# Kernel optimization log

Hardware: AMD Instinct MI355X
Metric: run time of the kernel (lower is better)

The kernel has to match this reference:

```python
import jax, jax.numpy as jnp
import numpy as np

L, D, HID, NH, E, K, P, IMG, NC, B = 4, 384, 1536, 6, 8, 2, 16, 224, 1000, 8
S = (IMG // P) ** 2 + 1  # 197 tokens (cls + patches)
EPS = 1e-5


def setup_inputs() -> dict:
    ks = iter(jax.random.split(jax.random.key(0), 32))
    g = lambda shape, s=0.02: jax.random.normal(next(ks), shape, jnp.float32) * s
    pd = 3 * P * P
    return dict(
        x=jax.random.normal(next(ks), (B, 3, IMG, IMG), jnp.float32),
        patch_w=g((pd, D)), patch_b=g((D,)),
        cls_tok=g((1, 1, D)), pos=g((1, S, D)),
        qkv_w=g((L, D, 3 * D)), qkv_b=g((L, 3 * D)),
        proj_w=g((L, D, D)), proj_b=g((L, D)),
        ln1_g=jnp.ones((L, D)), ln1_b=jnp.zeros((L, D)),
        ln2_g=jnp.ones((L, D)), ln2_b=jnp.zeros((L, D)),
        router_w=g((L, D, E)), router_b=g((L, E)),
        w1=g((L, E, D, HID)), b1=g((L, E, HID)),
        w2=g((L, E, HID, D)), b2=g((L, E, D)),
        norm_g=jnp.ones((D,)), norm_b=jnp.zeros((D,)),
        fc_w=g((D, NC)), fc_b=g((NC,)),
    )


def _ln(x, g, b):
    m = x.mean(-1, keepdims=True)
    v = ((x - m) ** 2).mean(-1, keepdims=True)
    return (x - m) * jax.lax.rsqrt(v + EPS) * g + b


def _mha(x, wqkv, bqkv, wo, bo):
    Bx, Sx, Dx = x.shape
    hd = Dx // NH
    qkv = x @ wqkv + bqkv
    q, k, v = jnp.split(qkv, 3, axis=-1)
    q = q.reshape(Bx, Sx, NH, hd)
    k = k.reshape(Bx, Sx, NH, hd)
    v = v.reshape(Bx, Sx, NH, hd)
    att = jnp.einsum('bqhd,bkhd->bhqk', q, k) / jnp.sqrt(jnp.float32(hd))
    att = jax.nn.softmax(att, axis=-1)
    o = jnp.einsum('bhqk,bkhd->bqhd', att, v).reshape(Bx, Sx, Dx)
    return o @ wo + bo


def _moe(x, rw, rb, w1, b1, w2, b2, noise):
    # Faithful to the masked-dense SparseMoE: non-routed experts see zeros,
    # so occupied experts leak expert_j(0)=gelu(b1_j)@W2_j+b2_j to all tokens.
    xf = x.reshape(-1, x.shape[-1])                     # [T, D]
    logits = xf @ rw + rb + noise * 0.01                # noisy gating
    vals, idx = jax.lax.top_k(logits, K)                # [T, K]
    gates = jax.nn.softmax(vals, axis=-1)               # [T, K]
    h = jax.nn.gelu(jnp.einsum('td,edh->teh', xf, w1) + b1[None], approximate=False)
    y = jnp.einsum('teh,ehd->ted', h, w2) + b2[None]    # [T, E, D]
    bias0 = jnp.einsum('eh,ehd->ed', jax.nn.gelu(b1, approximate=False), w2) + b2  # expert_j(0)
    oh = jax.nn.one_hot(idx, E, dtype=xf.dtype)         # [T, K, E]
    occ = (oh.sum(0) > 0).astype(xf.dtype)              # [K, E] slot occupancy (mask.sum()>0)
    bias_sum = occ @ bias0                              # [K, D]
    y_sel = jnp.take_along_axis(y, idx[:, :, None], axis=1)  # [T, K, D]
    out = jnp.einsum('tk,tkd->td', gates, y_sel - bias0[idx] + bias_sum[None])
    return out.reshape(x.shape)


def reference(x, patch_w, patch_b, cls_tok, pos, qkv_w, qkv_b, proj_w, proj_b,
              ln1_g, ln1_b, ln2_g, ln2_b, router_w, router_b,
              w1, b1, w2, b2, norm_g, norm_b, fc_w, fc_b):
    Bx = x.shape[0]
    Hp = IMG // P
    # torch unfold patchify: (B,C,Hp,Wp,p,p) -> (B, N, C*p*p), channel-major features
    patches = x.reshape(Bx, 3, Hp, P, Hp, P).transpose(0, 2, 4, 1, 3, 5).reshape(Bx, Hp * Hp, 3 * P * P)
    t = patches @ patch_w + patch_b
    t = jnp.concatenate([jnp.broadcast_to(cls_tok, (Bx, 1, D)), t], axis=1) + pos
    nkey = jax.random.key(42)
    for l in range(L):
        a = _mha(t, qkv_w[l], qkv_b[l], proj_w[l], proj_b[l])
        t = _ln(t + a, ln1_g[l], ln1_b[l])
        noise = jax.random.normal(jax.random.fold_in(nkey, l), (Bx * S, E), t.dtype)
        m = _moe(t, router_w[l], router_b[l], w1[l], b1[l], w2[l], b2[l], noise)
        t = _ln(t + m, ln2_g[l], ln2_b[l])
    t = _ln(t, norm_g, norm_b)
    return t[:, 0] @ fc_w + fc_b
```

## Files before the change

### kernel.cpp

```cpp
#include <hip/hip_runtime.h>
#include <hip/hip_bf16.h>

constexpr int LYR  = 4;
constexpr int DM   = 384;
constexpr int HIDN = 1536;
constexpr int NHEAD = 6;
constexpr int HDIM = 64;
constexpr int NEXP = 8;
constexpr int SEQ  = 197;
constexpr int BATCH = 8;
constexpr int TOK  = BATCH * SEQ;
constexpr int NCLS = 1000;
constexpr int CAPE = TOK;
constexpr int NPATCH = BATCH * 196;
constexpr float EPSLN = 1e-5f;
constexpr int KP = 40;

typedef __attribute__((ext_vector_type(8))) short short8v;
typedef __attribute__((ext_vector_type(4))) short short4v;
typedef __attribute__((ext_vector_type(2))) short short2v;
typedef __attribute__((ext_vector_type(4))) float f32x4v;

__host__ __device__ inline void tf2x32(unsigned k0, unsigned k1, unsigned x0, unsigned x1,
                                       unsigned& y0, unsigned& y1) {
  unsigned ks2 = k0 ^ k1 ^ 0x1BD11BDAu;
  unsigned v0 = x0 + k0, v1 = x1 + k1;
#define TFR(r) { v0 += v1; v1 = (v1 << (r)) | (v1 >> (32 - (r))); v1 ^= v0; }
  TFR(13) TFR(15) TFR(26) TFR(6)
  v0 += k1;  v1 += ks2 + 1u;
  TFR(17) TFR(29) TFR(16) TFR(24)
  v0 += ks2; v1 += k0 + 2u;
  TFR(13) TFR(15) TFR(26) TFR(6)
  v0 += k0;  v1 += k1 + 3u;
  TFR(17) TFR(29) TFR(16) TFR(24)
  v0 += k1;  v1 += ks2 + 4u;
  TFR(13) TFR(15) TFR(26) TFR(6)
  v0 += ks2; v1 += k0 + 5u;
#undef TFR
  y0 = v0; y1 = v1;
}

__device__ inline float erfinv32(float x) {
  float w = -log1pf(-x * x);
  float p;
  if (w < 5.f) {
    w -= 2.5f;
    p = 2.81022636e-08f;
    p = fmaf(p, w, 3.43273939e-07f);
    p = fmaf(p, w, -3.5233877e-06f);
    p = fmaf(p, w, -4.39150654e-06f);
    p = fmaf(p, w, 0.00021858087f);
    p = fmaf(p, w, -0.00125372503f);
    p = fmaf(p, w, -0.00417768164f);
    p = fmaf(p, w, 0.246640727f);
    p = fmaf(p, w, 1.50140941f);
  } else {
    w = sqrtf(w) - 3.f;
    p = -0.000200214257f;
    p = fmaf(p, w, 0.000100950558f);
    p = fmaf(p, w, 0.00134934322f);
    p = fmaf(p, w, -0.00367342844f);
    p = fmaf(p, w, 0.00573950773f);
    p = fmaf(p, w, -0.0076224613f);
    p = fmaf(p, w, 0.00943887047f);
    p = fmaf(p, w, 1.00167406f);
    p = fmaf(p, w, 2.83297682f);
  }
  return p * x;
}

__device__ inline float gelu_f(float x) {
  return 0.5f * x * (1.f + erff(x * 0.70710678118654752f));
}

__device__ inline unsigned short bf16_rne(float x) {
  unsigned u = __float_as_uint(x);
  unsigned r = (u + 0x7fffu + ((u >> 16) & 1u)) >> 16;
  return (unsigned short)r;
}
__device__ inline void split2(float x, short& hs, short& ls) {
  unsigned hu = bf16_rne(x);
  float hf = __uint_as_float(hu << 16);
  unsigned lu = bf16_rne(x - hf);
  hs = (short)hu; ls = (short)lu;
}

__global__ __launch_bounds__(256) void convw_kernel(const float* __restrict__ src,
                                                    short* __restrict__ dst,
                                                    int K, int N,
                                                    long srcLS, long dstLS) {
  const int nrg = N >> 6;
  const int rg = blockIdx.x;
  const int kr = rg / nrg, nr = rg - kr * nrg;
  const long eoffS = (long)blockIdx.z * srcLS + (long)blockIdx.y * K * N;
  const int nchunks = (K >> 5) * (N >> 4);
  const long eoffD = (long)blockIdx.z * dstLS + (long)blockIdx.y * (long)nchunks * 1024;
  __shared__ float st[64][65];
  const int tid = threadIdx.x;
  {
    const int c = (tid & 15) << 2;
    const int r0 = tid >> 4;
    const float* sp = src + eoffS + (long)(kr * 64) * N + nr * 64;
#pragma unroll
    for (int p = 0; p < 4; ++p) {
      const int r = p * 16 + r0;
      const float4 v = *(const float4*)&sp[(long)r * N + c];
      st[r][c] = v.x; st[r][c + 1] = v.y; st[r][c + 2] = v.z; st[r][c + 3] = v.w;
    }
  }
  __syncthreads();
  const int lane = tid & 63;
  const int wch = tid >> 6;
  const int nloc0 = lane & 15, kg = lane >> 4;
#pragma unroll
  for (int q = 0; q < 2; ++q) {
    const int ch = wch + q * 4;
    const int kt2 = ch >> 2, nt2 = ch & 3;
    const int kl = kt2 * 32 + kg * 8;
    const int nl = nt2 * 16 + nloc0;
    short8v hv, lv;
#pragma unroll
    for (int j = 0; j < 8; j++) {
      short h, l; split2(st[kl + j][nl], h, l);
      hv[j] = h; lv[j] = l;
    }
    const int ktg = kr * 2 + kt2, ntg = nr * 4 + nt2;
    const long chunk = (long)ktg * (N >> 4) + ntg;
    *(short8v*)&dst[eoffD + chunk * 1024 + lane * 8] = hv;
    *(short8v*)&dst[eoffD + chunk * 1024 + 512 + lane * 8] = lv;
  }
}

template <int KTOT, int NTOT, int MODE>
__global__ __launch_bounds__(256) void gemm_lds_kernel(
    const short* __restrict__ Ah, const short* __restrict__ Al,
    const short* __restrict__ Wf, const float* __restrict__ bias,
    const int* __restrict__ lists, const int* __restrict__ counts,
    float* __restrict__ outF, short* __restrict__ outH, short* __restrict__ outL) {
  constexpr bool ISMOE = (MODE == 1 || MODE == 2);
  constexpr bool SPLITOUT = (MODE == 1 || MODE == 3);
  constexpr int SPE = NTOT / 64;
  constexpr int NK = KTOT / 64;
  constexpr int PIT = 72;
  const int strip = blockIdx.x;
  int e, c0;
  if (ISMOE) { e = strip / SPE; c0 = (strip - e * SPE) * 64; }
  else { e = 0; c0 = strip * 64; if (c0 >= NTOT) return; }
  const int m = blockIdx.y;
  const int cnt = ISMOE ? counts[e] : TOK;
  if (m * 64 >= cnt) return;
  const int rowsM = min(64, cnt - m * 64);
  __shared__ int ent[64];
  __shared__ short sh[2][64 * PIT];
  __shared__ short sl[2][64 * PIT];
  const int tid = threadIdx.x;
  const int w = tid >> 6, lane = tid & 63;
  if (ISMOE) {
    if (tid < 64) ent[tid] = (tid < rowsM) ? lists[e * CAPE + m * 64 + tid] : -1;
    __syncthreads();
  }
  const int sr = tid >> 2, skq = (tid & 3) * 8;
  bool okr; long arow = 0;
  if (!ISMOE) {
    okr = (sr < rowsM);
    arow = (long)(m * 64 + (okr ? sr : 0)) * KTOT;
  } else {
    const int pid = ent[sr];
    okr = (pid >= 0);
    arow = (long)(okr ? ((MODE == 1) ? (pid >> 1) : pid) : 0) * KTOT;
  }
  const short* W = Wf + (long)e * ((KTOT >> 5) * (NTOT >> 4)) * 1024;
  const int wm = (w >> 1) * 32, wn = (w & 1) * 32;
  f32x4v Cr[2][2] = {};
  short8v c0h, c1h, c0l, c1l;
#pragma unroll
  for (int j = 0; j < 8; j++) { c0h[j] = 0; c1h[j] = 0; c0l[j] = 0; c1l[j] = 0; }
  if (okr) {
    c0h = *(const short8v*)&Ah[arow + skq];
    c1h = *(const short8v*)&Ah[arow + 32 + skq];
    c0l = *(const short8v*)&Al[arow + skq];
    c1l = *(const short8v*)&Al[arow + 32 + skq];
  }
  for (int kt = 0; kt < NK; ++kt) {
    const int cb = kt & 1;
    *(short8v*)&sh[cb][sr * PIT + skq] = c0h;
    *(short8v*)&sh[cb][sr * PIT + 32 + skq] = c1h;
    *(short8v*)&sl[cb][sr * PIT + skq] = c0l;
    *(short8v*)&sl[cb][sr * PIT + 32 + skq] = c1l;
    if (kt + 1 < NK && okr) {
      const long ab = arow + (kt + 1) * 64;
      c0h = *(const short8v*)&Ah[ab + skq];
      c1h = *(const short8v*)&Ah[ab + 32 + skq];
      c0l = *(const short8v*)&Al[ab + skq];
      c1l = *(const short8v*)&Al[ab + 32 + skq];
    }
    short8v wh[2][2], wl[2][2];
#pragma unroll
    for (int kk = 0; kk < 2; ++kk) {
      const long wkb = ((long)(kt * 2 + kk) * (NTOT >> 4) + (c0 >> 4) + (wn >> 4)) * 1024;
#pragma unroll
      for (int nt = 0; nt < 2; ++nt) {
        wh[kk][nt] = *(const short8v*)&W[wkb + nt * 1024 + lane * 8];
        wl[kk][nt] = *(const short8v*)&W[wkb + nt * 1024 + 512 + lane * 8];
      }
    }
    __syncthreads();
#pragma unroll
    for (int kk = 0; kk < 2; ++kk) {
      short8v bh[2], bl[2];
#pragma unroll
      for (int tt = 0; tt < 2; ++tt) {
        const int trow = wm + tt * 16 + (lane & 15);
        bh[tt] = *(const short8v*)&sh[cb][trow * PIT + kk * 32 + (lane >> 4) * 8];
        bl[tt] = *(const short8v*)&sl[cb][trow * PIT + kk * 32 + (lane >> 4) * 8];
      }
#pragma unroll
      for (int nt = 0; nt < 2; ++nt) {
#pragma unroll
        for (int tt = 0; tt < 2; ++tt) {
          Cr[tt][nt] = __builtin_amdgcn_mfma_f32_16x16x32_bf16(wh[kk][nt], bh[tt], Cr[tt][nt], 0, 0, 0);
          Cr[tt][nt] = __builtin_amdgcn_mfma_f32_16x16x32_bf16(wh[kk][nt], bl[tt], Cr[tt][nt], 0, 0, 0);
          Cr[tt][nt] = __builtin_amdgcn_mfma_f32_16x16x32_bf16(wl[kk][nt], bh[tt], Cr[tt][nt], 0, 0, 0);
        }
      }
    }
  }
  const int tl = lane & 15;
  const int nq = (lane >> 4) * 4;
#pragma unroll
  for (int tt = 0; tt < 2; ++tt) {
    const int trow = wm + tt * 16 + tl;
    if (trow < rowsM) {
      const long orow = (long)(ISMOE ? ent[trow] : (m * 64 + trow)) * NTOT;
#pragma unroll
      for (int nt = 0; nt < 2; ++nt) {
        const int n = c0 + wn + nt * 16 + nq;
        const float4 bv = *(const float4*)&bias[(ISMOE ? e * NTOT : 0) + n];
        float o0 = Cr[tt][nt][0] + bv.x, o1 = Cr[tt][nt][1] + bv.y;
        float o2 = Cr[tt][nt][2] + bv.z, o3 = Cr[tt][nt][3] + bv.w;
        if (SPLITOUT) {
          if (MODE == 1) { o0 = gelu_f(o0); o1 = gelu_f(o1); o2 = gelu_f(o2); o3 = gelu_f(o3); }
          short4v hv, lv; short hs, ls;
          split2(o0, hs, ls); hv[0] = hs; lv[0] = ls;
          split2(o1, hs, ls); hv[1] = hs; lv[1] = ls;
          split2(o2, hs, ls); hv[2] = hs; lv[2] = ls;
          split2(o3, hs, ls); hv[3] = hs; lv[3] = ls;
          *(short4v*)&outH[orow + n] = hv;
          *(short4v*)&outL[orow + n] = lv;
        } else {
          *(float4*)&outF[orow + n] = make_float4(o0, o1, o2, o3);
        }
      }
    }
  }
}

__global__ __launch_bounds__(256) void patch_mfma_kernel(const float* __restrict__ x,
                                                         const short* __restrict__ Wf,
                                                         const float* __restrict__ pb,
                                                         const float* __restrict__ pos,
                                                         float* __restrict__ t,
                                                         short* __restrict__ tfh,
                                                         short* __restrict__ tfl) {
  constexpr int KTOT = 768, NTOT = DM;
  const int rowsM = min(64, NPATCH - (int)blockIdx.x * 64);
  const int c0 = blockIdx.z * 64;
  const int tid = threadIdx.x;
  const int w = tid >> 6, lane = tid & 63;
  __shared__ short xh[64 * KP];
  __shared__ short xl[64 * KP];
  const int sr = tid >> 2, skq = (tid & 3) * 8;
  const bool okr = (sr < rowsM);
  const int p = blockIdx.x * 64 + sr;
  const int pbat = okr ? (p / 196) : 0;
  const int pn = okr ? (p - pbat * 196) : 0;
  const int hp = pn / 14, wp = pn - hp * 14;
  const float* xbase = x + ((long)pbat * 3 * 224 + hp * 16) * 224 + wp * 16;
  const int wm = (w >> 1) * 32, wn = (w & 1) * 32;
  f32x4v Cr[2][2] = {};
  float4 ra = make_float4(0.f, 0.f, 0.f, 0.f), rb = ra;
  if (okr) {
    const int f = skq;
    const int c = f >> 8, py = (f >> 4) & 15, px = f & 15;
    const float* ptr = xbase + ((long)c * 224 + py) * 224 + px;
    ra = *(const float4*)ptr;
    rb = *(const float4*)(ptr + 4);
  }
  for (int kt = 0; kt < KTOT / 32; ++kt) {
    __syncthreads();
    {
      const float v[8] = {ra.x, ra.y, ra.z, ra.w, rb.x, rb.y, rb.z, rb.w};
      short8v hv, lv;
#pragma unroll
      for (int j = 0; j < 8; j++) { short h, l; split2(v[j], h, l); hv[j] = h; lv[j] = l; }
      *(short8v*)&xh[sr * KP + skq] = hv;
      *(short8v*)&xl[sr * KP + skq] = lv;
    }
    if (kt + 1 < KTOT / 32 && okr) {
      const int f = (kt + 1) * 32 + skq;
      const int c = f >> 8, py = (f >> 4) & 15, px = f & 15;
      const float* ptr = xbase + ((long)c * 224 + py) * 224 + px;
      ra = *(const float4*)ptr;
      rb = *(const float4*)(ptr + 4);
    }
    __syncthreads();
    short8v bhv[2], blv[2];
#pragma unroll
    for (int tt = 0; tt < 2; ++tt) {
      const int trow = wm + tt * 16 + (lane & 15);
      bhv[tt] = *(const short8v*)&xh[trow * KP + (lane >> 4) * 8];
      blv[tt] = *(const short8v*)&xl[trow * KP + (lane >> 4) * 8];
    }
    const long wkb = ((long)kt * (NTOT >> 4) + (c0 >> 4) + (wn >> 4)) * 1024;
#pragma unroll
    for (int nt = 0; nt < 2; ++nt) {
      const short8v wh = *(const short8v*)&Wf[wkb + nt * 1024 + lane * 8];
      const short8v wl = *(const short8v*)&Wf[wkb + nt * 1024 + 512 + lane * 8];
#pragma unroll
      for (int tt = 0; tt < 2; ++tt) {
        Cr[tt][nt] = __builtin_amdgcn_mfma_f32_16x16x32_bf16(wh, bhv[tt], Cr[tt][nt], 0, 0, 0);
        Cr[tt][nt] = __builtin_amdgcn_mfma_f32_16x16x32_bf16(wh, blv[tt], Cr[tt][nt], 0, 0, 0);
        Cr[tt][nt] = __builtin_amdgcn_mfma_f32_16x16x32_bf16(wl, bhv[tt], Cr[tt][nt], 0, 0, 0);
      }
    }
  }
  const int tl = lane & 15;
  const int nq = (lane >> 4) * 4;
#pragma unroll
  for (int tt = 0; tt < 2; ++tt) {
    const int trow = wm + tt * 16 + tl;
    if (trow < rowsM) {
      const int r = blockIdx.x * 64 + trow;
      const int b2 = r / 196, n2 = r - b2 * 196;
      const long orow = (long)(b2 * SEQ + 1 + n2) * DM;
#pragma unroll
      for (int nt = 0; nt < 2; ++nt) {
        const int n = c0 + wn + nt * 16 + nq;
        const float4 bv = *(const float4*)&pb[n];
        const float4 pv = *(const float4*)&pos[(1 + n2) * DM + n];
        float o0 = Cr[tt][nt][0] + bv.x + pv.x;
        float o1 = Cr[tt][nt][1] + bv.y + pv.y;
        float o2 = Cr[tt][nt][2] + bv.z + pv.z;
        float o3 = Cr[tt][nt][3] + bv.w + pv.w;
        *(float4*)&t[orow + n] = make_float4(o0, o1, o2, o3);
        short4v hv, lv; short hs, ls;
        split2(o0, hs, ls); hv[0] = hs; lv[0] = ls;
        split2(o1, hs, ls); hv[1] = hs; lv[1] = ls;
        split2(o2, hs, ls); hv[2] = hs; lv[2] = ls;
        split2(o3, hs, ls); hv[3] = hs; lv[3] = ls;
        *(short4v*)&tfh[orow + n] = hv;
        *(short4v*)&tfl[orow + n] = lv;
      }
    }
  }
}

__global__ void cls_pos_kernel(const float* __restrict__ cls, const float* __restrict__ pos,
                               float* __restrict__ t,
                               short* __restrict__ tfh, short* __restrict__ tfl) {
  int b = blockIdx.x, d = threadIdx.x;
  float v = cls[d] + pos[d];
  t[(b * SEQ) * DM + d] = v;
  short hs, ls; split2(v, hs, ls);
  tfh[(b * SEQ) * DM + d] = hs;
  tfl[(b * SEQ) * DM + d] = ls;
}

constexpr int APIT = 232;
constexpr int VPIT = 40;
__global__ __launch_bounds__(256) void attn_mfma_kernel(const short* __restrict__ qh,
                                                        const short* __restrict__ ql,
                                                        short* __restrict__ afh,
                                                        short* __restrict__ afl) {
  const int bh = blockIdx.x;
  const int b = bh / NHEAD, h = bh % NHEAD;
  const int q0 = blockIdx.y * 64;
  const int tid = threadIdx.x;
  const int w = tid >> 6, lane = tid & 63;
  const int tl = lane & 15, g = lane >> 4;
  __shared__ short ph[4][16 * APIT];
  __shared__ short pl[4][16 * APIT];
  __shared__ short vsh[64 * VPIT];
  __shared__ short vsl[64 * VPIT];
  const long hq = (long)h * HDIM;

  const int qrow = q0 + w * 16 + tl;
  const long qtok = (long)(b * SEQ + min(qrow, SEQ - 1)) * 1152;
  short8v qfh[2], qfl[2];
#pragma unroll
  for (int s = 0; s < 2; ++s) {
    qfh[s] = *(const short8v*)&qh[qtok + hq + s * 32 + g * 8];
    qfl[s] = *(const short8v*)&ql[qtok + hq + s * 32 + g * 8];
  }

  f32x4v sc[13];
#pragma unroll
  for (int n = 0; n < 13; ++n) {
    f32x4v acc = {};
    const long ktok = (long)(b * SEQ + min(n * 16 + tl, SEQ - 1)) * 1152;
#pragma unroll
    for (int s = 0; s < 2; ++s) {
      const short8v kh = *(const short8v*)&qh[ktok + DM + hq + s * 32 + g * 8];
      const short8v kl = *(const short8v*)&ql[ktok + DM + hq + s * 32 + g * 8];
      acc = __builtin_amdgcn_mfma_f32_16x16x32_bf16(kh, qfh[s], acc, 0, 0, 0);
      acc = __builtin_amdgcn_mfma_f32_16x16x32_bf16(kh, qfl[s], acc, 0, 0, 0);
      acc = __builtin_amdgcn_mfma_f32_16x16x32_bf16(kl, qfh[s], acc, 0, 0, 0);
    }
    sc[n] = acc;
  }

  float m = -1e30f;
#pragma unroll
  for (int n = 0; n < 13; ++n)
#pragma unroll
    for (int j = 0; j < 4; ++j) {
      const int key = n * 16 + g * 4 + j;
      float v = sc[n][j] * 0.125f;
      v = (key < SEQ) ? v : -1e30f;
      sc[n][j] = v;
      m = fmaxf(m, v);
    }
  m = fmaxf(m, __shfl_xor(m, 16));
  m = fmaxf(m, __shfl_xor(m, 32));
  float sum = 0.f;
#pragma unroll
  for (int n = 0; n < 13; ++n)
#pragma unroll
    for (int j = 0; j < 4; ++j) {
      float p = __expf(sc[n][j] - m);
      sc[n][j] = p; sum += p;
    }
  sum += __shfl_xor(sum, 16);
  sum += __shfl_xor(sum, 32);
  const float inv = 1.f / sum;

  short* prowh = &ph[w][tl * APIT];
  short* prowl = &pl[w][tl * APIT];
#pragma unroll
  for (int n = 0; n < 13; ++n) {
    short4v hv, lv;
#pragma unroll
    for (int j = 0; j < 4; ++j) {
      short hs, ls; split2(sc[n][j] * inv, hs, ls);
      hv[j] = hs; lv[j] = ls;
    }
    *(short4v*)&prowh[n * 16 + g * 4] = hv;
    *(short4v*)&prowl[n * 16 + g * 4] = lv;
  }
  {
    short4v z; z[0] = 0; z[1] = 0; z[2] = 0; z[3] = 0;
    *(short4v*)&prowh[208 + g * 4] = z;
    *(short4v*)&prowl[208 + g * 4] = z;
  }

  const int kp = (tid & 15) * 2;
  const int dg = (tid >> 4) * 4;
  f32x4v oacc[4] = {};
  short4v r0h, r0l, r1h, r1l;
  {
    const long t0 = (long)(b * SEQ + min(kp, SEQ - 1)) * 1152 + 2 * DM + hq + dg;
    const long t1 = (long)(b * SEQ + min(kp + 1, SEQ - 1)) * 1152 + 2 * DM + hq + dg;
    r0h = *(const short4v*)&qh[t0]; r0l = *(const short4v*)&ql[t0];
    r1h = *(const short4v*)&qh[t1]; r1l = *(const short4v*)&ql[t1];
  }
  for (int st = 0; st < 7; ++st) {
    __syncthreads();
#pragma unroll
    for (int jj = 0; jj < 4; ++jj) {
      short2v h2; h2[0] = r0h[jj]; h2[1] = r1h[jj];
      short2v l2; l2[0] = r0l[jj]; l2[1] = r1l[jj];
      *(short2v*)&vsh[(dg + jj) * VPIT + kp] = h2;
      *(short2v*)&vsl[(dg + jj) * VPIT + kp] = l2;
    }
    if (st + 1 < 7) {
      const int kb = (st + 1) * 32;
      const long t0 = (long)(b * SEQ + min(kb + kp, SEQ - 1)) * 1152 + 2 * DM + hq + dg;
      const long t1 = (long)(b * SEQ + min(kb + kp + 1, SEQ - 1)) * 1152 + 2 * DM + hq + dg;
      r0h = *(const short4v*)&qh[t0]; r0l = *(const short4v*)&ql[t0];
      r1h = *(const short4v*)&qh[t1]; r1l = *(const short4v*)&ql[t1];
    }
    __syncthreads();
    const short8v pbh = *(const short8v*)&prowh[st * 32 + g * 8];
    const short8v pbl = *(const short8v*)&prowl[st * 32 + g * 8];
#pragma unroll
    for (int dt = 0; dt < 4; ++dt) {
      const short8v vfh = *(const short8v*)&vsh[(dt * 16 + tl) * VPIT + g * 8];
      const short8v vfl = *(const short8v*)&vsl[(dt * 16 + tl) * VPIT + g * 8];
      oacc[dt] = __builtin_amdgcn_mfma_f32_16x16x32_bf16(vfh, pbh, oacc[dt], 0, 0, 0);
      oacc[dt] = __builtin_amdgcn_mfma_f32_16x16x32_bf16(vfh, pbl, oacc[dt], 0, 0, 0);
      oacc[dt] = __builtin_amdgcn_mfma_f32_16x16x32_bf16(vfl, pbh, oacc[dt], 0, 0, 0);
    }
  }

  if (qrow < SEQ) {
    const long obase = (long)(b * SEQ + qrow) * DM + hq;
#pragma unroll
    for (int dt = 0; dt < 4; ++dt) {
      short4v hv, lv; short hs, ls;
      split2(oacc[dt][0], hs, ls); hv[0] = hs; lv[0] = ls;
      split2(oacc[dt][1], hs, ls); hv[1] = hs; lv[1] = ls;
      split2(oacc[dt][2], hs, ls); hv[2] = hs; lv[2] = ls;
      split2(oacc[dt][3], hs, ls); hv[3] = hs; lv[3] = ls;
      *(short4v*)&afh[obase + dt * 16 + g * 4] = hv;
      *(short4v*)&afl[obase + dt * 16 + g * 4] = lv;
    }
  }
}

__global__ __launch_bounds__(384) void add_ln_router_kernel(float* __restrict__ t,
                                                            const float* __restrict__ delta,
                                                            const float* __restrict__ g,
                                                            const float* __restrict__ bta,
                                                            short* __restrict__ tfh,
                                                            short* __restrict__ tfl,
                                                            const float* __restrict__ rw,
                                                            const float* __restrict__ rb,
                                                            unsigned k0, unsigned k1,
                                                            float* __restrict__ gates,
                                                            int* __restrict__ idxb) {
  const int tok = blockIdx.x, d = threadIdx.x;
  __shared__ float yb[DM];
  __shared__ float rs[6], rq[6];
  float v = t[tok * DM + d] + delta[tok * DM + d];
  float sv = v, sq = v * v;
  for (int off = 32; off > 0; off >>= 1) { sv += __shfl_xor(sv, off); sq += __shfl_xor(sq, off); }
  int w = d >> 6, ln = d & 63;
  if (ln == 0) { rs[w] = sv; rq[w] = sq; }
  __syncthreads();
  float mean = 0.f, ms = 0.f;
#pragma unroll
  for (int i = 0; i < 6; i++) { mean += rs[i]; ms += rq[i]; }
  mean *= (1.f / DM); ms *= (1.f / DM);
  float inv = rsqrtf(ms - mean * mean + EPSLN);
  float y = (v - mean) * inv * g[d] + bta[d];
  t[tok * DM + d] = y;
  yb[d] = y;
  short hs, ls; split2(y, hs, ls);
  tfh[tok * DM + d] = hs;
  tfl[tok * DM + d] = ls;
  __syncthreads();
  if (d < 64) {
    const int e = d & 7, j = d >> 3;
    float acc = 0.f;
    for (int d2 = j * 48; d2 < j * 48 + 48; d2++) acc += yb[d2] * rw[d2 * NEXP + e];
    acc += __shfl_xor(acc, 8);
    acc += __shfl_xor(acc, 16);
    acc += __shfl_xor(acc, 32);
    if (d < 8) {
      acc += rb[e];
      unsigned i = (unsigned)(tok * NEXP + e);
      unsigned y0, y1;
      tf2x32(k0, k1, 0u, i, y0, y1);
      unsigned bits = y0 ^ y1;
      float f = __uint_as_float(0x3f800000u | (bits >> 9)) - 1.0f;
      const float lo = -0.99999994f;
      float u = f * 2.0f + lo;
      u = fmaxf(lo, u);
      acc += 0.01f * (1.41421356f * erfinv32(u));
    }
    float lg[8];
#pragma unroll
    for (int qq = 0; qq < 8; qq++) lg[qq] = __shfl(acc, qq);
    if (d == 0) {
      int i0 = 0; float v0 = lg[0];
#pragma unroll
      for (int qq = 1; qq < 8; qq++) if (lg[qq] > v0) { v0 = lg[qq]; i0 = qq; }
      int i1 = -1; float v1 = -1e30f;
#pragma unroll
      for (int qq = 0; qq < 8; qq++) if (qq != i0 && lg[qq] > v1) { v1 = lg[qq]; i1 = qq; }
      float e1 = __expf(v1 - v0);
      float g0 = 1.f / (1.f + e1);
      idxb[tok * 2] = i0; idxb[tok * 2 + 1] = i1;
      gates[tok * 2] = g0; gates[tok * 2 + 1] = 1.f - g0;
    }
  }
}

__global__ __launch_bounds__(1024) void bucket_kernel(const int* __restrict__ idxb,
                                                      int* __restrict__ lists,
                                                      int* __restrict__ counts,
                                                      const float* __restrict__ bias0,
                                                      float* __restrict__ bias_sum) {
  __shared__ int lc[NEXP];
  __shared__ int locc[2 * NEXP];
  const int tid = threadIdx.x;
  if (tid < NEXP) lc[tid] = 0;
  if (tid < 2 * NEXP) locc[tid] = 0;
  __syncthreads();
  for (int i = tid; i < 2 * TOK; i += 1024) {
    const int e = idxb[i];
    const int p = atomicAdd(&lc[e], 1);
    lists[e * CAPE + p] = i;
    locc[(i & 1) * NEXP + e] = 1;
  }
  __syncthreads();
  if (tid < NEXP) counts[tid] = lc[tid];
  if (tid < 2 * DM) {
    const int k = tid / DM, d = tid - k * DM;
    float acc = 0.f;
#pragma unroll
    for (int e = 0; e < NEXP; e++)
      if (locc[k * NEXP + e]) acc += bias0[e * DM + d];
    bias_sum[k * DM + d] = acc;
  }
}

__global__ void prep_kernel(const float* __restrict__ b2, float* __restrict__ bias0) {
  const long i = ((long)blockIdx.y * NEXP + blockIdx.x) * DM + threadIdx.x;
  bias0[i] = b2[i];
}

__global__ __launch_bounds__(384) void bias0_partial_kernel(const float* __restrict__ b1,
                                                            const float* __restrict__ w2,
                                                            float* __restrict__ bias0) {
  const int e = blockIdx.x, kc = blockIdx.y, l = blockIdx.z;
  __shared__ float gb[128];
  const int tid = threadIdx.x;
  if (tid < 128) gb[tid] = gelu_f(b1[(long)l * NEXP * HIDN + e * HIDN + kc * 128 + tid]);
  __syncthreads();
  float acc = 0.f;
  const float* W = w2 + ((long)l * NEXP * HIDN + (long)e * HIDN + kc * 128) * DM + tid;
  for (int j2 = 0; j2 < 128; j2++) acc += gb[j2] * W[(long)j2 * DM];
  atomicAdd(&bias0[((long)l * NEXP + e) * DM + tid], acc);
}

__global__ __launch_bounds__(384) void moe_combine_ln_kernel(float* __restrict__ t,
                                                             const float* __restrict__ ybuf,
                                                             const float* __restrict__ gates,
                                                             const int* __restrict__ idxb,
                                                             const float* __restrict__ bias0,
                                                             const float* __restrict__ bias_sum,
                                                             const float* __restrict__ g,
                                                             const float* __restrict__ bta,
                                                             short* __restrict__ tfh,
                                                             short* __restrict__ tfl) {
  int tok = blockIdx.x, d = threadIdx.x;
  float g0 = gates[tok * 2], g1 = gates[tok * 2 + 1];
  int i0 = idxb[tok * 2], i1 = idxb[tok * 2 + 1];
  float m0 = ybuf[(tok * 2) * DM + d] - bias0[i0 * DM + d] + bias_sum[d];
  float m1 = ybuf[(tok * 2 + 1) * DM + d] - bias0[i1 * DM + d] + bias_sum[DM + d];
  float v = t[tok * DM + d] + g0 * m0 + g1 * m1;
  float sv = v, sq = v * v;
  for (int off = 32; off > 0; off >>= 1) { sv += __shfl_xor(sv, off); sq += __shfl_xor(sq, off); }
  __shared__ float rs[6], rq[6];
  int w = d >> 6, ln = d & 63;
  if (ln == 0) { rs[w] = sv; rq[w] = sq; }
  __syncthreads();
  float mean = 0.f, ms = 0.f;
#pragma unroll
  for (int i = 0; i < 6; i++) { mean += rs[i]; ms += rq[i]; }
  mean *= (1.f / DM); ms *= (1.f / DM);
  float inv = rsqrtf(ms - mean * mean + EPSLN);
  float y = (v - mean) * inv * g[d] + bta[d];
  t[tok * DM + d] = y;
  short hs, ls; split2(y, hs, ls);
  tfh[tok * DM + d] = hs;
  tfl[tok * DM + d] = ls;
}

__global__ __launch_bounds__(256) void final_kernel(const float* __restrict__ t,
                                                    const float* __restrict__ ng,
                                                    const float* __restrict__ nb,
                                                    const float* __restrict__ fw,
                                                    const float* __restrict__ fb,
                                                    float* __restrict__ out) {
  int b = blockIdx.x, chunk = blockIdx.y, tid = threadIdx.x;
  __shared__ float xr[DM];
  __shared__ float rs[4], rq[4];
  const float* row = t + (b * SEQ) * DM;
  float sv = 0.f, sq = 0.f;
  for (int i = tid; i < DM; i += 256) { float x = row[i]; xr[i] = x; sv += x; sq += x * x; }
  for (int off = 32; off > 0; off >>= 1) { sv += __shfl_xor(sv, off); sq += __shfl_xor(sq, off); }
  int w = tid >> 6, ln = tid & 63;
  if (ln == 0) { rs[w] = sv; rq[w] = sq; }
  __syncthreads();
  float mean = (rs[0] + rs[1] + rs[2] + rs[3]) * (1.f / DM);
  float ms = (rq[0] + rq[1] + rq[2] + rq[3]) * (1.f / DM);
  float inv = rsqrtf(ms - mean * mean + EPSLN);
  for (int i = tid; i < DM; i += 256) xr[i] = (xr[i] - mean) * inv * ng[i] + nb[i];
  __syncthreads();
  int c = chunk * 250 + tid;
  if (tid < 250) {
    float acc = fb[c];
    for (int k = 0; k < DM; k++) acc += xr[k] * fw[k * NCLS + c];
    out[b * NCLS + c] = acc;
  }
}

extern "C" void kernel_launch(void* const* d_in, const int* in_sizes, int n_in,
                              void* d_out, int out_size, void* d_ws, size_t ws_size,
                              hipStream_t stream) {
  const float* x       = (const float*)d_in[0];
  const float* patch_w = (const float*)d_in[1];
  const float* patch_b = (const float*)d_in[2];
  const float* cls_tok = (const float*)d_in[3];
  const float* pos     = (const float*)d_in[4];
  const float* qkv_w   = (const float*)d_in[5];
  const float* qkv_b   = (const float*)d_in[6];
  const float* proj_w  = (const float*)d_in[7];
  const float* proj_b  = (const float*)d_in[8];
  const float* ln1_g   = (const float*)d_in[9];
  const float* ln1_b   = (const float*)d_in[10];
  const float* ln2_g   = (const float*)d_in[11];
  const float* ln2_b   = (const float*)d_in[12];
  const float* router_w = (const float*)d_in[13];
  const float* router_b = (const float*)d_in[14];
  const float* w1      = (const float*)d_in[15];
  const float* b1      = (const float*)d_in[16];
  const float* w2      = (const float*)d_in[17];
  const float* b2      = (const float*)d_in[18];
  const float* norm_g  = (const float*)d_in[19];
  const float* norm_b  = (const float*)d_in[20];
  const float* fc_w    = (const float*)d_in[21];
  const float* fc_b    = (const float*)d_in[22];

  float* ws = (float*)d_ws;
  float* t        = ws;
  float* proj     = t + TOK * DM;
  float* ybuf     = proj + TOK * DM;
  float* bias0    = ybuf + TOK * 2 * DM;
  float* bias_sum = bias0 + LYR * NEXP * DM;
  float* gates    = bias_sum + 2 * DM;
  int* idxb   = (int*)(gates + TOK * 2);
  int* lists  = idxb + TOK * 2;
  int* counts = lists + NEXP * CAPE;
  short* tfh = (short*)(counts + 8);
  short* tfl = tfh + TOK * DM;
  short* afh = tfl + TOK * DM;
  short* afl = afh + TOK * DM;
  short* qvh = afl + TOK * DM;
  short* qvl = qvh + TOK * 1152;
  short* hbh = qvl + TOK * 1152;
  short* hbl = hbh + 2 * TOK * HIDN;
  short* wqf = hbl + 2 * TOK * HIDN;
  short* wpf = wqf + (long)LYR * 864 * 1024;
  short* w1f = wpf + (long)LYR * 288 * 1024;
  short* w2f = w1f + (long)LYR * NEXP * 1152 * 1024;
  short* wpatf = w2f + (long)LYR * NEXP * 1152 * 1024;

  convw_kernel<<<dim3(72, 1, 1), 256, 0, stream>>>(patch_w, wpatf, 768, DM, 0, 0);
  convw_kernel<<<dim3(108, 1, LYR), 256, 0, stream>>>(qkv_w, wqf, DM, 1152,
                                                      (long)DM * 1152, 864L * 1024);
  convw_kernel<<<dim3(36, 1, LYR), 256, 0, stream>>>(proj_w, wpf, DM, DM,
                                                     (long)DM * DM, 288L * 1024);
  convw_kernel<<<dim3(144, NEXP, LYR), 256, 0, stream>>>(w1, w1f, DM, HIDN,
                                                         (long)NEXP * DM * HIDN,
                                                         (long)NEXP * 1152 * 1024);
  convw_kernel<<<dim3(144, NEXP, LYR), 256, 0, stream>>>(w2, w2f, HIDN, DM,
                                                         (long)NEXP * HIDN * DM,
                                                         (long)NEXP * 1152 * 1024);
  prep_kernel<<<dim3(NEXP, LYR), DM, 0, stream>>>(b2, bias0);
  bias0_partial_kernel<<<dim3(NEXP, 12, LYR), 384, 0, stream>>>(b1, w2, bias0);

  patch_mfma_kernel<<<dim3(25, 1, 6), 256, 0, stream>>>(x, wpatf, patch_b, pos, t, tfh, tfl);
  cls_pos_kernel<<<BATCH, DM, 0, stream>>>(cls_tok, pos, t, tfh, tfl);

  for (int l = 0; l < LYR; l++) {
    const short* wqf_l = wqf + (long)l * 864 * 1024;
    const short* wpf_l = wpf + (long)l * 288 * 1024;
    const short* w1f_l = w1f + (long)l * NEXP * 1152 * 1024;
    const short* w2f_l = w2f + (long)l * NEXP * 1152 * 1024;
    const float* bias0_l = bias0 + (long)l * NEXP * DM;

    gemm_lds_kernel<DM, 1152, 3><<<dim3(24, 25), 256, 0, stream>>>(
        tfh, tfl, wqf_l, qkv_b + l * 1152, nullptr, nullptr, nullptr, qvh, qvl);
    attn_mfma_kernel<<<dim3(BATCH * NHEAD, 4), 256, 0, stream>>>(qvh, qvl, afh, afl);
    gemm_lds_kernel<DM, DM, 0><<<dim3(8, 25), 256, 0, stream>>>(
        afh, afl, wpf_l, proj_b + l * DM, nullptr, nullptr, proj, nullptr, nullptr);

    unsigned kl0, kl1;
    tf2x32(0u, 42u, 0u, (unsigned)l, kl0, kl1);
    add_ln_router_kernel<<<TOK, DM, 0, stream>>>(
        t, proj, ln1_g + l * DM, ln1_b + l * DM, tfh, tfl,
        router_w + l * DM * NEXP, router_b + l * NEXP, kl0, kl1, gates, idxb);
    bucket_kernel<<<1, 1024, 0, stream>>>(idxb, lists, counts, bias0_l, bias_sum);
    gemm_lds_kernel<DM, HIDN, 1><<<dim3(192, 25), 256, 0, stream>>>(
        tfh, tfl, w1f_l, b1 + l * NEXP * HIDN, lists, counts, nullptr, hbh, hbl);
    gemm_lds_kernel<HIDN, DM, 2><<<dim3(48, 25), 256, 0, stream>>>(
        hbh, hbl, w2f_l, b2 + l * NEXP * DM, lists, counts, ybuf, nullptr, nullptr);
    moe_combine_ln_kernel<<<TOK, DM, 0, stream>>>(t, ybuf, gates, idxb, bias0_l, bias_sum,
                                                  ln2_g + l * DM, ln2_b + l * DM, tfh, tfl);
  }

  final_kernel<<<dim3(BATCH, 4), 256, 0, stream>>>(t, norm_g, norm_b, fc_w, fc_b,
                                                   (float*)d_out);
}
```

Before: 825.5 us.

## Merge weight-conversion launches, fold cls into patch kernel, fuse bucketing into router

All weight-conversion launches and the b2 copy are merged into one flat-grid kernel, and the cls+pos token write becomes an extra block row of the patch GEMM. The per-layer single-block bucket kernel is removed: the router kernel appends tokens to expert lists with global atomics and sets occupancy flags. The combine kernel now sums the bias of occupied experts itself, and the QKV GEMM zeroes counts and occ for the layer. This cuts launch count and removes a serial one-block stage each layer, at the cost of nondeterministic list order and global atomic contention.

```diff
diff --git a/kernel.cpp b/kernel.cpp
--- a/kernel.cpp
+++ b/kernel.cpp
@@ -85,22 +85,40 @@
   hs = (short)hu; ls = (short)lu;
 }
 
-__global__ __launch_bounds__(256) void convw_kernel(const float* __restrict__ src,
-                                                    short* __restrict__ dst,
-                                                    int K, int N,
-                                                    long srcLS, long dstLS) {
+__global__ __launch_bounds__(256) void convw_all_kernel(
+    const float* __restrict__ pw, const float* __restrict__ qw,
+    const float* __restrict__ prw, const float* __restrict__ w1,
+    const float* __restrict__ w2, const float* __restrict__ b2,
+    short* __restrict__ wpatf, short* __restrict__ wqf, short* __restrict__ wpf,
+    short* __restrict__ w1f, short* __restrict__ w2f, float* __restrict__ bias0) {
+  const int id = blockIdx.x;
+  if (id >= 9864) {
+    for (int i = threadIdx.x; i < LYR * NEXP * DM; i += 256) bias0[i] = b2[i];
+    return;
+  }
+  const float* src; short* dst; int K, N, rg;
+  if (id < 72) { src = pw; dst = wpatf; K = 768; N = DM; rg = id; }
+  else if (id < 504) {
+    const int t2 = id - 72; const int l = t2 / 108; rg = t2 - l * 108;
+    src = qw + (long)l * DM * 1152; dst = wqf + (long)l * 864 * 1024; K = DM; N = 1152;
+  } else if (id < 648) {
+    const int t2 = id - 504; const int l = t2 / 36; rg = t2 - l * 36;
+    src = prw + (long)l * DM * DM; dst = wpf + (long)l * 288 * 1024; K = DM; N = DM;
+  } else if (id < 5256) {
+    const int t2 = id - 648; const int le = t2 / 144; rg = t2 - le * 144;
+    src = w1 + (long)le * DM * HIDN; dst = w1f + (long)le * 1152 * 1024; K = DM; N = HIDN;
+  } else {
+    const int t2 = id - 5256; const int le = t2 / 144; rg = t2 - le * 144;
+    src = w2 + (long)le * HIDN * DM; dst = w2f + (long)le * 1152 * 1024; K = HIDN; N = DM;
+  }
   const int nrg = N >> 6;
-  const int rg = blockIdx.x;
   const int kr = rg / nrg, nr = rg - kr * nrg;
-  const long eoffS = (long)blockIdx.z * srcLS + (long)blockIdx.y * K * N;
-  const int nchunks = (K >> 5) * (N >> 4);
-  const long eoffD = (long)blockIdx.z * dstLS + (long)blockIdx.y * (long)nchunks * 1024;
   __shared__ float st[64][65];
   const int tid = threadIdx.x;
   {
     const int c = (tid & 15) << 2;
     const int r0 = tid >> 4;
-    const float* sp = src + eoffS + (long)(kr * 64) * N + nr * 64;
+    const float* sp = src + (long)(kr * 64) * N + nr * 64;
 #pragma unroll
     for (int p = 0; p < 4; ++p) {
       const int r = p * 16 + r0;
@@ -126,8 +144,8 @@
     }
     const int ktg = kr * 2 + kt2, ntg = nr * 4 + nt2;
     const long chunk = (long)ktg * (N >> 4) + ntg;
-    *(short8v*)&dst[eoffD + chunk * 1024 + lane * 8] = hv;
-    *(short8v*)&dst[eoffD + chunk * 1024 + 512 + lane * 8] = lv;
+    *(short8v*)&dst[chunk * 1024 + lane * 8] = hv;
+    *(short8v*)&dst[chunk * 1024 + 512 + lane * 8] = lv;
   }
 }
 
@@ -136,12 +154,15 @@
     const short* __restrict__ Ah, const short* __restrict__ Al,
     const short* __restrict__ Wf, const float* __restrict__ bias,
     const int* __restrict__ lists, const int* __restrict__ counts,
-    float* __restrict__ outF, short* __restrict__ outH, short* __restrict__ outL) {
+    float* __restrict__ outF, short* __restrict__ outH, short* __restrict__ outL,
+    int* __restrict__ zeroBuf) {
   constexpr bool ISMOE = (MODE == 1 || MODE == 2);
   constexpr bool SPLITOUT = (MODE == 1 || MODE == 3);
   constexpr int SPE = NTOT / 64;
   constexpr int NK = KTOT / 64;
   constexpr int PIT = 72;
+  if (zeroBuf && blockIdx.x == 0 && blockIdx.y == 0 && threadIdx.x < 24)
+    zeroBuf[threadIdx.x] = 0;
   const int strip = blockIdx.x;
   int e, c0;
   if (ISMOE) { e = strip / SPE; c0 = (strip - e * SPE) * 64; }
@@ -259,12 +280,26 @@
                                                          const short* __restrict__ Wf,
                                                          const float* __restrict__ pb,
                                                          const float* __restrict__ pos,
+                                                         const float* __restrict__ cls,
                                                          float* __restrict__ t,
                                                          short* __restrict__ tfh,
                                                          short* __restrict__ tfl) {
   constexpr int KTOT = 768, NTOT = DM;
+  const int c0 = blockIdx.z * 64;
+  if (blockIdx.x == 25) {
+#pragma unroll
+    for (int p = 0; p < 2; ++p) {
+      const int i = threadIdx.x + p * 256;
+      const int b = i >> 6, d = c0 + (i & 63);
+      const float v = cls[d] + pos[d];
+      t[(b * SEQ) * DM + d] = v;
+      short hs, ls; split2(v, hs, ls);
+      tfh[(b * SEQ) * DM + d] = hs;
+      tfl[(b * SEQ) * DM + d] = ls;
+    }
+    return;
+  }
   const int rowsM = min(64, NPATCH - (int)blockIdx.x * 64);
-  const int c0 = blockIdx.z * 64;
   const int tid = threadIdx.x;
   const int w = tid >> 6, lane = tid & 63;
   __shared__ short xh[64 * KP];
@@ -355,17 +390,6 @@
   }
 }
 
-__global__ void cls_pos_kernel(const float* __restrict__ cls, const float* __restrict__ pos,
-                               float* __restrict__ t,
-                               short* __restrict__ tfh, short* __restrict__ tfl) {
-  int b = blockIdx.x, d = threadIdx.x;
-  float v = cls[d] + pos[d];
-  t[(b * SEQ) * DM + d] = v;
-  short hs, ls; split2(v, hs, ls);
-  tfh[(b * SEQ) * DM + d] = hs;
-  tfl[(b * SEQ) * DM + d] = ls;
-}
-
 constexpr int APIT = 232;
 constexpr int VPIT = 40;
 __global__ __launch_bounds__(256) void attn_mfma_kernel(const short* __restrict__ qh,
@@ -517,7 +541,10 @@
                                                             const float* __restrict__ rb,
                                                             unsigned k0, unsigned k1,
                                                             float* __restrict__ gates,
-                                                            int* __restrict__ idxb) {
+                                                            int* __restrict__ idxb,
+                                                            int* __restrict__ lists,
+                                                            int* __restrict__ counts,
+                                                            int* __restrict__ occ) {
   const int tok = blockIdx.x, d = threadIdx.x;
   __shared__ float yb[DM];
   __shared__ float rs[6], rq[6];
@@ -572,42 +599,14 @@
       float g0 = 1.f / (1.f + e1);
       idxb[tok * 2] = i0; idxb[tok * 2 + 1] = i1;
       gates[tok * 2] = g0; gates[tok * 2 + 1] = 1.f - g0;
-    }
-  }
-}
-
-__global__ __launch_bounds__(1024) void bucket_kernel(const int* __restrict__ idxb,
-                                                      int* __restrict__ lists,
-                                                      int* __restrict__ counts,
-                                                      const float* __restrict__ bias0,
-                                                      float* __restrict__ bias_sum) {
-  __shared__ int lc[NEXP];
-  __shared__ int locc[2 * NEXP];
-  const int tid = threadIdx.x;
-  if (tid < NEXP) lc[tid] = 0;
-  if (tid < 2 * NEXP) locc[tid] = 0;
-  __syncthreads();
-  for (int i = tid; i < 2 * TOK; i += 1024) {
-    const int e = idxb[i];
-    const int p = atomicAdd(&lc[e], 1);
-    lists[e * CAPE + p] = i;
-    locc[(i & 1) * NEXP + e] = 1;
-  }
-  __syncthreads();
-  if (tid < NEXP) counts[tid] = lc[tid];
-  if (tid < 2 * DM) {
-    const int k = tid / DM, d = tid - k * DM;
-    float acc = 0.f;
-#pragma unroll
-    for (int e = 0; e < NEXP; e++)
-      if (locc[k * NEXP + e]) acc += bias0[e * DM + d];
-    bias_sum[k * DM + d] = acc;
-  }
-}
-
-__global__ void prep_kernel(const float* __restrict__ b2, float* __restrict__ bias0) {
-  const long i = ((long)blockIdx.y * NEXP + blockIdx.x) * DM + threadIdx.x;
-  bias0[i] = b2[i];
+      const int p0 = atomicAdd(&counts[i0], 1);
+      lists[i0 * CAPE + p0] = tok * 2;
+      const int p1 = atomicAdd(&counts[i1], 1);
+      lists[i1 * CAPE + p1] = tok * 2 + 1;
+      occ[i0] = 1;
+      occ[8 + i1] = 1;
+    }
+  }
 }
 
 __global__ __launch_bounds__(384) void bias0_partial_kernel(const float* __restrict__ b1,
@@ -629,7 +628,7 @@
                                                              const float* __restrict__ gates,
                                                              const int* __restrict__ idxb,
                                                              const float* __restrict__ bias0,
-                                                             const float* __restrict__ bias_sum,
+                                                             const int* __restrict__ occ,
                                                              const float* __restrict__ g,
                                                              const float* __restrict__ bta,
                                                              short* __restrict__ tfh,
@@ -637,8 +636,15 @@
   int tok = blockIdx.x, d = threadIdx.x;
   float g0 = gates[tok * 2], g1 = gates[tok * 2 + 1];
   int i0 = idxb[tok * 2], i1 = idxb[tok * 2 + 1];
-  float m0 = ybuf[(tok * 2) * DM + d] - bias0[i0 * DM + d] + bias_sum[d];
-  float m1 = ybuf[(tok * 2 + 1) * DM + d] - bias0[i1 * DM + d] + bias_sum[DM + d];
+  float bs0 = 0.f, bs1 = 0.f;
+#pragma unroll
+  for (int e = 0; e < NEXP; e++) {
+    const float bv = bias0[e * DM + d];
+    if (occ[e]) bs0 += bv;
+    if (occ[8 + e]) bs1 += bv;
+  }
+  float m0 = ybuf[(tok * 2) * DM + d] - bias0[i0 * DM + d] + bs0;
+  float m1 = ybuf[(tok * 2 + 1) * DM + d] - bias0[i1 * DM + d] + bs1;
   float v = t[tok * DM + d] + g0 * m0 + g1 * m1;
   float sv = v, sq = v * v;
   for (int off = 32; off > 0; off >>= 1) { sv += __shfl_xor(sv, off); sq += __shfl_xor(sq, off); }
@@ -719,12 +725,12 @@
   float* proj     = t + TOK * DM;
   float* ybuf     = proj + TOK * DM;
   float* bias0    = ybuf + TOK * 2 * DM;
-  float* bias_sum = bias0 + LYR * NEXP * DM;
-  float* gates    = bias_sum + 2 * DM;
+  float* gates    = bias0 + LYR * NEXP * DM;
   int* idxb   = (int*)(gates + TOK * 2);
   int* lists  = idxb + TOK * 2;
   int* counts = lists + NEXP * CAPE;
-  short* tfh = (short*)(counts + 8);
+  int* occ    = counts + 8;
+  short* tfh = (short*)(occ + 16);
   short* tfl = tfh + TOK * DM;
   short* afh = tfl + TOK * DM;
   short* afl = afh + TOK * DM;
@@ -738,22 +744,11 @@
   short* w2f = w1f + (long)LYR * NEXP * 1152 * 1024;
   short* wpatf = w2f + (long)LYR * NEXP * 1152 * 1024;
 
-  convw_kernel<<<dim3(72, 1, 1), 256, 0, stream>>>(patch_w, wpatf, 768, DM, 0, 0);
-  convw_kernel<<<dim3(108, 1, LYR), 256, 0, stream>>>(qkv_w, wqf, DM, 1152,
-                                                      (long)DM * 1152, 864L * 1024);
-  convw_kernel<<<dim3(36, 1, LYR), 256, 0, stream>>>(proj_w, wpf, DM, DM,
-                                                     (long)DM * DM, 288L * 1024);
-  convw_kernel<<<dim3(144, NEXP, LYR), 256, 0, stream>>>(w1, w1f, DM, HIDN,
-                                                         (long)NEXP * DM * HIDN,
-                                                         (long)NEXP * 1152 * 1024);
-  convw_kernel<<<dim3(144, NEXP, LYR), 256, 0, stream>>>(w2, w2f, HIDN, DM,
-                                                         (long)NEXP * HIDN * DM,
-                                                         (long)NEXP * 1152 * 1024);
-  prep_kernel<<<dim3(NEXP, LYR), DM, 0, stream>>>(b2, bias0);
+  convw_all_kernel<<<9865, 256, 0, stream>>>(patch_w, qkv_w, proj_w, w1, w2, b2,
+                                             wpatf, wqf, wpf, w1f, w2f, bias0);
   bias0_partial_kernel<<<dim3(NEXP, 12, LYR), 384, 0, stream>>>(b1, w2, bias0);
-
-  patch_mfma_kernel<<<dim3(25, 1, 6), 256, 0, stream>>>(x, wpatf, patch_b, pos, t, tfh, tfl);
-  cls_pos_kernel<<<BATCH, DM, 0, stream>>>(cls_tok, pos, t, tfh, tfl);
+  patch_mfma_kernel<<<dim3(26, 1, 6), 256, 0, stream>>>(x, wpatf, patch_b, pos, cls_tok,
+                                                        t, tfh, tfl);
 
   for (int l = 0; l < LYR; l++) {
     const short* wqf_l = wqf + (long)l * 864 * 1024;
@@ -763,22 +758,22 @@
     const float* bias0_l = bias0 + (long)l * NEXP * DM;
 
     gemm_lds_kernel<DM, 1152, 3><<<dim3(24, 25), 256, 0, stream>>>(
-        tfh, tfl, wqf_l, qkv_b + l * 1152, nullptr, nullptr, nullptr, qvh, qvl);
+        tfh, tfl, wqf_l, qkv_b + l * 1152, nullptr, nullptr, nullptr, qvh, qvl, counts);
     attn_mfma_kernel<<<dim3(BATCH * NHEAD, 4), 256, 0, stream>>>(qvh, qvl, afh, afl);
     gemm_lds_kernel<DM, DM, 0><<<dim3(8, 25), 256, 0, stream>>>(
-        afh, afl, wpf_l, proj_b + l * DM, nullptr, nullptr, proj, nullptr, nullptr);
+        afh, afl, wpf_l, proj_b + l * DM, nullptr, nullptr, proj, nullptr, nullptr, nullptr);
 
     unsigned kl0, kl1;
     tf2x32(0u, 42u, 0u, (unsigned)l, kl0, kl1);
     add_ln_router_kernel<<<TOK, DM, 0, stream>>>(
         t, proj, ln1_g + l * DM, ln1_b + l * DM, tfh, tfl,
-        router_w + l * DM * NEXP, router_b + l * NEXP, kl0, kl1, gates, idxb);
-    bucket_kernel<<<1, 1024, 0, stream>>>(idxb, lists, counts, bias0_l, bias_sum);
+        router_w + l * DM * NEXP, router_b + l * NEXP, kl0, kl1, gates, idxb,
+        lists, counts, occ);
     gemm_lds_kernel<DM, HIDN, 1><<<dim3(192, 25), 256, 0, stream>>>(
-        tfh, tfl, w1f_l, b1 + l * NEXP * HIDN, lists, counts, nullptr, hbh, hbl);
+        tfh, tfl, w1f_l, b1 + l * NEXP * HIDN, lists, counts, nullptr, hbh, hbl, nullptr);
     gemm_lds_kernel<HIDN, DM, 2><<<dim3(48, 25), 256, 0, stream>>>(
-        hbh, hbl, w2f_l, b2 + l * NEXP * DM, lists, counts, ybuf, nullptr, nullptr);
-    moe_combine_ln_kernel<<<TOK, DM, 0, stream>>>(t, ybuf, gates, idxb, bias0_l, bias_sum,
+        hbh, hbl, w2f_l, b2 + l * NEXP * DM, lists, counts, ybuf, nullptr, nullptr, nullptr);
+    moe_combine_ln_kernel<<<TOK, DM, 0, stream>>>(t, ybuf, gates, idxb, bias0_l, occ,
                                                   ln2_g + l * DM, ln2_b + l * DM, tfh, tfl);
   }
 
```

Result: slower. 1.254 ms (+51.9%).
